# Kernel optimization log

Measured on AMD Instinct MI355X. Metric: run time of the kernel, lower is better.

The kernel has to match this reference:

```python
import jax, jax.numpy as jnp
import numpy as np

B, S, D, N = 8, 4096, 1024, 64
EPS = 1e-5


def setup_inputs() -> dict:
    key = jax.random.key(0)
    ks = jax.random.split(key, 6)
    sD = 1.0 / np.sqrt(D)
    sN = 1.0 / np.sqrt(N)
    return {
        "x": jax.random.normal(ks[0], (B, S, D), dtype=jnp.float32),
        "ln_w": jnp.ones((D,), jnp.float32),
        "ln_b": jnp.zeros((D,), jnp.float32),
        "Wi": jax.random.normal(ks[1], (N, D), jnp.float32) * sD,
        "bi": jnp.zeros((N,), jnp.float32),
        "Wf": jax.random.normal(ks[2], (N, D), jnp.float32) * sD,
        "bf": jnp.zeros((N,), jnp.float32),
        "Wz": jax.random.normal(ks[3], (N, D), jnp.float32) * sD,
        "bz": jnp.zeros((N,), jnp.float32),
        "Wo": jax.random.normal(ks[4], (N, D), jnp.float32) * sD,
        "bo": jnp.zeros((N,), jnp.float32),
        "Wp": jax.random.normal(ks[5], (D, N), jnp.float32) * sN,
        "bp": jnp.zeros((D,), jnp.float32),
    }


def reference(x, ln_w, ln_b, Wi, bi, Wf, bf, Wz, bz, Wo, bo, Wp, bp):
    # LayerNorm over last dim (eps matches torch default 1e-5)
    mu = jnp.mean(x, axis=-1, keepdims=True)
    var = jnp.mean(jnp.square(x - mu), axis=-1, keepdims=True)
    xn = (x - mu) * jax.lax.rsqrt(var + EPS) * ln_w + ln_b

    # Precompute all four projections as batched GEMMs: (B,S,N)
    log_i = jnp.clip(jnp.einsum('bsd,nd->bsn', xn, Wi) + bi, -20.0, 20.0)
    log_f = jnp.clip(jnp.einsum('bsd,nd->bsn', xn, Wf) + bf, -20.0, 20.0)
    z = jnp.tanh(jnp.einsum('bsd,nd->bsn', xn, Wz) + bz)
    o = jax.nn.sigmoid(jnp.einsum('bsd,nd->bsn', xn, Wo) + bo)

    # Stabilized exponential-gated recurrence via lax.scan over time
    def step(carry, inp):
        c, m = carry
        li, lf, zt, ot = inp
        m_new = jnp.maximum(m + lf, li)
        i_s = jnp.exp(li - m_new)
        f_s = jnp.exp(m + lf - m_new)
        c = f_s * c + i_s * zt
        h = ot * jnp.tanh(c)
        return (c, m_new), h

    c0 = jnp.zeros((x.shape[0], log_i.shape[-1]), x.dtype)
    m0 = jnp.zeros_like(c0)
    # time-major inputs: (S,B,N)
    tm = lambda a: jnp.swapaxes(a, 0, 1)
    _, h_seq = jax.lax.scan(step, (c0, m0), (tm(log_i), tm(log_f), tm(z), tm(o)))
    h_seq = jnp.swapaxes(h_seq, 0, 1)  # (B,S,N)

    return jnp.einsum('bsn,dn->bsd', h_seq, Wp) + bp
```

## Files before the change

### kernel.cpp

```cpp
#include <hip/hip_runtime.h>
#include <hip/hip_bf16.h>

#define BB 8
#define SS 4096
#define DD 1024
#define NN 64
#define ROWS (BB * SS)
#define GLD 256
#define NCHUNK 256
#define CLEN 16

typedef _Float16 f16;
using f16x8 = __attribute__((ext_vector_type(8))) _Float16;
using f32x4 = __attribute__((ext_vector_type(4))) float;

__global__ __launch_bounds__(256) void prep_all(const float* __restrict__ Wi, const float* __restrict__ bi,
                                                const float* __restrict__ Wf, const float* __restrict__ bfv,
                                                const float* __restrict__ Wz, const float* __restrict__ bz,
                                                const float* __restrict__ Wo, const float* __restrict__ bo,
                                                const float* __restrict__ Wp,
                                                const float* __restrict__ ln_w, const float* __restrict__ ln_b,
                                                f16* __restrict__ Wpk, f16* __restrict__ Wpf,
                                                float* __restrict__ ball, float* __restrict__ e_all) {
    if (blockIdx.x < 384) {
        int i = blockIdx.x * 256 + threadIdx.x;
        if (i < 32768) {
            int l = i & 63, cb = (i >> 6) & 15, s = i >> 10;
            int r = cb * 16 + (l & 15);
            int c = s * 32 + (l >> 4) * 8;
            int g = r >> 6, rem = r & 63;
            const float* W = (g == 0) ? Wi : (g == 1) ? Wf : (g == 2) ? Wz : Wo;
            const float* src = W + rem * 1024 + c;
            const float* lwp = ln_w + c;
            f16x8 v;
            #pragma unroll
            for (int e = 0; e < 8; ++e) v[e] = (f16)(src[e] * lwp[e]);
            *reinterpret_cast<f16x8*>(Wpk + (size_t)s * 8192 + cb * 512 + l * 8) = v;
        } else if (i < 32768 + 65536) {
            int j = i - 32768;
            Wpf[j] = (f16)Wp[j];
        }
    } else {
        int j = (blockIdx.x - 384) * 4 + (threadIdx.x >> 6);
        int lane = threadIdx.x & 63;
        int g = j >> 6, rem = j & 63;
        const float* W  = (g == 0) ? Wi : (g == 1) ? Wf : (g == 2) ? Wz : Wo;
        const float* bs = (g == 0) ? bi : (g == 1) ? bfv : (g == 2) ? bz : bo;
        const float* row = W + rem * 1024;
        float d = 0.0f, e = 0.0f;
        #pragma unroll
        for (int t = 0; t < 16; ++t) {
            int k = lane + 64 * t;
            float w = row[k];
            e += ln_w[k] * w;
            d += ln_b[k] * w;
        }
        #pragma unroll
        for (int off = 1; off < 64; off <<= 1) {
            e += __shfl_xor(e, off);
            d += __shfl_xor(d, off);
        }
        if (lane == 0) { ball[j] = bs[rem] + d; e_all[j] = e; }
    }
}

__global__ __launch_bounds__(512, 1) void gate_gemm(const float* __restrict__ x,
                                                    const f16* __restrict__ Wpk,
                                                    const float* __restrict__ ball,
                                                    const float* __restrict__ e_all,
                                                    float* __restrict__ gates,
                                                    float4* __restrict__ s4) {
    int bm = blockIdx.x * 128;
    int tid = threadIdx.x;
    int wid = tid >> 6, lane = tid & 63;
    int wm = wid >> 2, wn = wid & 3;
    int lrow = lane & 15, lkg = lane >> 4;
    int srow = tid >> 2, skg = tid & 3;

    __shared__ __align__(16) char ldsbuf[98304];
    __shared__ float2 stats_lds[128];

    const float4* xrow = reinterpret_cast<const float4*>(x + (size_t)(bm + srow) * DD) + skg * 4;
    float4 A0, A1, A2, A3, B0, B1, B2, B3;
    uint4 W0, W1, W2, W3;
    const uint4* wsrc = reinterpret_cast<const uint4*>(Wpk) + wid * 256 + lane;

    auto loadA = [&](int s) { const float4* p = xrow + s * 16; A0 = p[0]; A1 = p[1]; A2 = p[2]; A3 = p[3]; };
    auto loadB = [&](int s) { const float4* p = xrow + s * 16; B0 = p[0]; B1 = p[1]; B2 = p[2]; B3 = p[3]; };
    auto loadW = [&](int s) { const uint4* p = wsrc + (size_t)s * 2048; W0 = p[0]; W1 = p[64]; W2 = p[128]; W3 = p[192]; };
    auto writeW = [&](int buf) {
        uint4* d = reinterpret_cast<uint4*>(ldsbuf + buf * 32768 + wid * 4096) + lane;
        d[0] = W0; d[64] = W1; d[128] = W2; d[192] = W3;
    };

    float s1 = 0.0f, s2 = 0.0f;
    auto writeXv = [&](float4 v0, float4 v1, float4 v2, float4 v3, int buf) {
        float xv[16] = {v0.x, v0.y, v0.z, v0.w, v1.x, v1.y, v1.z, v1.w,
                        v2.x, v2.y, v2.z, v2.w, v3.x, v3.y, v3.z, v3.w};
        f16x8 p0, p1;
        #pragma unroll
        for (int e = 0; e < 8; ++e) {
            s1 += xv[e] + xv[8 + e];
            s2 += xv[e] * xv[e] + xv[8 + e] * xv[8 + e];
            p0[e] = (f16)xv[e];
            p1[e] = (f16)xv[8 + e];
        }
        char* base = ldsbuf + 65536 + buf * 16384 + srow * 128;
        int r7 = srow & 7;
        *reinterpret_cast<f16x8*>(base + 16 * ((2 * skg) ^ r7))     = p0;
        *reinterpret_cast<f16x8*>(base + 16 * ((2 * skg + 1) ^ r7)) = p1;
    };

    f32x4 acc[4][4] = {};
    auto compute = [&](int buf) {
        #pragma unroll
        for (int h = 0; h < 2; ++h) {
            f16x8 a[4];
            #pragma unroll
            for (int mf = 0; mf < 4; ++mf) {
                int row = wm * 64 + mf * 16 + lrow;
                a[mf] = *reinterpret_cast<const f16x8*>(
                    ldsbuf + 65536 + buf * 16384 + row * 128 + 16 * ((4 * h + lkg) ^ (row & 7)));
            }
            #pragma unroll
            for (int nf = 0; nf < 4; ++nf) {
                int cb = wn * 4 + nf;
                f16x8 w = *reinterpret_cast<const f16x8*>(
                    ldsbuf + buf * 32768 + h * 16384 + cb * 1024 + lane * 16);
                #pragma unroll
                for (int mf = 0; mf < 4; ++mf)
                    acc[mf][nf] = __builtin_amdgcn_mfma_f32_16x16x32_f16(a[mf], w, acc[mf][nf], 0, 0, 0);
            }
        }
    };
    auto stepSync = [&]() {
        asm volatile("s_waitcnt lgkmcnt(0)" ::: "memory");
        __builtin_amdgcn_s_barrier();
        __builtin_amdgcn_sched_barrier(0);
    };

    loadA(0); loadB(1); loadW(0);
    writeW(0);
    writeXv(A0, A1, A2, A3, 0);
    loadA(2); loadW(1);
    stepSync();

    for (int it = 0; it < 8; ++it) {
        int s = 2 * it;
        compute(0);
        writeW(1);
        writeXv(B0, B1, B2, B3, 1);
        if (s + 2 <= 15) loadW(s + 2);
        if (s + 3 <= 15) loadB(s + 3);
        stepSync();
        compute(1);
        if (s + 2 <= 15) {
            writeW(0);
            writeXv(A0, A1, A2, A3, 0);
        }
        if (s + 3 <= 15) loadW(s + 3);
        if (s + 4 <= 15) loadA(s + 4);
        stepSync();
    }

    s1 += __shfl_xor(s1, 1); s2 += __shfl_xor(s2, 1);
    s1 += __shfl_xor(s1, 2); s2 += __shfl_xor(s2, 2);
    if ((tid & 3) == 0) {
        float mu = s1 * (1.0f / DD);
        float var = s2 * (1.0f / DD) - mu * mu;
        float rsd = rsqrtf(var + 1e-5f);
        float2 st; st.x = mu * rsd; st.y = rsd;
        stats_lds[srow] = st;
    }
    __syncthreads();

    float* glds = reinterpret_cast<float*>(ldsbuf);
    int c0 = wn * 64;
    int rb = (lane >> 4) * 4;
    #pragma unroll
    for (int mf = 0; mf < 4; ++mf) {
        #pragma unroll
        for (int nf = 0; nf < 4; ++nf) {
            int col = c0 + nf * 16 + (lane & 15);
            float bc = ball[col];
            float ec = e_all[col];
            #pragma unroll
            for (int r = 0; r < 4; ++r) {
                int rl = wm * 64 + mf * 16 + rb + r;
                float2 st = stats_lds[rl];
                float v = acc[mf][nf][r] * st.y + bc - st.x * ec;
                float res;
                if (wn == 0 || wn == 1)      res = fminf(fmaxf(v, -20.0f), 20.0f);
                else if (wn == 2)            res = tanhf(v);
                else                         res = 1.0f / (1.0f + expf(-v));
                gates[(size_t)(bm + rl) * GLD + col] = res;
                if (wn < 3)
                    glds[rl * 192 + col] = res;
            }
        }
    }
    __syncthreads();

    int b = bm >> 12;
    int cb0 = (bm & 4095) >> 4;
    {
        int lr0 = wid * 16;
        float Lf = 0.0f, m = -1e30f, c = 0.0f;
        #pragma unroll
        for (int j = 0; j < 16; ++j) {
            const float* g = glds + (lr0 + j) * 192;
            float li = g[lane], lf = g[64 + lane], z = g[128 + lane];
            Lf += lf;
            float ma = m + lf;
            float mn = fmaxf(ma, li);
            c = __expf(ma - mn) * c + __expf(li - mn) * z;
            m = mn;
        }
        float4 v; v.x = Lf; v.y = m; v.z = c; v.w = 0.0f;
        s4[(size_t)(b * NCHUNK + cb0 + wid) * 64 + lane] = v;
    }
}

__global__ __launch_bounds__(64) void scan_b(const float4* __restrict__ s4,
                                             float2* __restrict__ c2) {
    int b = blockIdx.x;
    int n = threadIdx.x;
    size_t base = (size_t)b * NCHUNK * 64 + n;
    float c = 0.0f, m = 0.0f;
    float4 cur[16];
    #pragma unroll
    for (int d = 0; d < 16; ++d) cur[d] = s4[base + (size_t)d * 64];
    for (int kb = 0; kb < NCHUNK; kb += 16) {
        float4 nxt[16];
        if (kb + 16 < NCHUNK) {
            #pragma unroll
            for (int d = 0; d < 16; ++d) nxt[d] = s4[base + (size_t)(kb + 16 + d) * 64];
        }
        #pragma unroll
        for (int d = 0; d < 16; ++d) {
            float2 ci; ci.x = m; ci.y = c;
            c2[base + (size_t)(kb + d) * 64] = ci;
            float4 v = cur[d];
            float ma = m + v.x;
            float mo = fmaxf(ma, v.y);
            c = expf(ma - mo) * c + expf(v.y - mo) * v.z;
            m = mo;
        }
        #pragma unroll
        for (int d = 0; d < 16; ++d) cur[d] = nxt[d];
    }
}

__global__ __launch_bounds__(256) void out_fused(const float* __restrict__ gates,
                                                 const float2* __restrict__ c2,
                                                 const f16* __restrict__ Wpf,
                                                 const float* __restrict__ bp,
                                                 float* __restrict__ out) {
    int tid = threadIdx.x, wid = tid >> 6, lane = tid & 63;
    int r0 = blockIdx.x * 32;
    int b = r0 >> 12;
    int k0 = (r0 & 4095) >> 4;

    __shared__ __align__(16) f16 hlds[32 * 64];

    if (wid < 2) {
        int k = k0 + wid;
        float2 ci = c2[((size_t)b * NCHUNK + k) * 64 + lane];
        float m = ci.x, c = ci.y;
        const float* gp = gates + (size_t)(r0 + wid * 16) * GLD + lane;
        #pragma unroll
        for (int t = 0; t < 16; ++t) {
            float li = gp[0], lf = gp[64], z = gp[128], o = gp[192];
            gp += GLD;
            float ma = m + lf;
            float mn = fmaxf(ma, li);
            c = __expf(ma - mn) * c + __expf(li - mn) * z;
            m = mn;
            int row = wid * 16 + t;
            hlds[row * 64 + (((lane >> 3) ^ (row & 7)) << 3) + (lane & 7)] = (f16)(o * tanhf(c));
        }
    }
    __syncthreads();

    int c0 = wid * 256;
    int lrow = lane & 15, lkg = lane >> 4;
    f32x4 acc[2][16] = {};
    #pragma unroll
    for (int ks = 0; ks < 2; ++ks) {
        int kk = ks * 32;
        f16x8 a[2];
        #pragma unroll
        for (int mf = 0; mf < 2; ++mf) {
            int row = mf * 16 + lrow;
            int slot = (kk >> 3) + lkg;
            a[mf] = *reinterpret_cast<const f16x8*>(&hlds[row * 64 + ((slot ^ (row & 7)) << 3)]);
        }
        #pragma unroll
        for (int nf = 0; nf < 16; ++nf) {
            f16x8 bfr = *reinterpret_cast<const f16x8*>(Wpf + (size_t)(c0 + nf * 16 + lrow) * NN + kk + lkg * 8);
            #pragma unroll
            for (int mf = 0; mf < 2; ++mf)
                acc[mf][nf] = __builtin_amdgcn_mfma_f32_16x16x32_f16(a[mf], bfr, acc[mf][nf], 0, 0, 0);
        }
    }
    int rb = lkg * 4;
    #pragma unroll
    for (int nf = 0; nf < 16; ++nf) {
        int col = c0 + nf * 16 + lrow;
        float bias = bp[col];
        #pragma unroll
        for (int mf = 0; mf < 2; ++mf) {
            #pragma unroll
            for (int r = 0; r < 4; ++r) {
                int row = r0 + mf * 16 + rb + r;
                out[(size_t)row * DD + col] = acc[mf][nf][r] + bias;
            }
        }
    }
}

extern "C" void kernel_launch(void* const* d_in, const int* in_sizes, int n_in,
                              void* d_out, int out_size, void* d_ws, size_t ws_size,
                              hipStream_t stream) {
    const float* x    = (const float*)d_in[0];
    const float* ln_w = (const float*)d_in[1];
    const float* ln_b = (const float*)d_in[2];
    const float* Wi   = (const float*)d_in[3];
    const float* bi   = (const float*)d_in[4];
    const float* Wf   = (const float*)d_in[5];
    const float* bfv  = (const float*)d_in[6];
    const float* Wz   = (const float*)d_in[7];
    const float* bz   = (const float*)d_in[8];
    const float* Wo   = (const float*)d_in[9];
    const float* bo   = (const float*)d_in[10];
    const float* Wp   = (const float*)d_in[11];
    const float* bp   = (const float*)d_in[12];
    float* out = (float*)d_out;

    char* w = (char*)d_ws;
    float* gates = (float*)w;  w += (size_t)ROWS * GLD * 4;
    float4* s4   = (float4*)w; w += (size_t)BB * NCHUNK * 64 * 16;
    float2* c2   = (float2*)w; w += (size_t)BB * NCHUNK * 64 * 8;
    f16* Wpk     = (f16*)w;    w += 32 * 8192 * 2;
    f16* Wpf     = (f16*)w;    w += 1024 * 64 * 2;
    float* ball  = (float*)w;  w += 256 * 4;
    float* e_all = (float*)w;  w += 256 * 4;

    prep_all<<<448, 256, 0, stream>>>(Wi, bi, Wf, bfv, Wz, bz, Wo, bo, Wp,
                                      ln_w, ln_b, Wpk, Wpf, ball, e_all);
    gate_gemm<<<ROWS / 128, 512, 0, stream>>>(x, Wpk, ball, e_all, gates, s4);
    scan_b<<<BB, 64, 0, stream>>>(s4, c2);
    out_fused<<<ROWS / 32, 256, 0, stream>>>(gates, c2, Wpf, bp, out);
}
```

Measured before the change: 136.5 us.

## Split fused scan-and-output kernel into separate chunk-scan and output GEMM kernels

Replaces the fused out_fused kernel, where two of four waves ran the per-chunk recurrence into LDS before all waves did the output projection, with two kernels. scan_c runs the recurrence for each chunk and writes h to a new f16 workspace buffer. out_gemm then reads h from global memory and runs MFMA over half-width column tiles, launching twice as many blocks. This removes the idle waves during the serial scan phase and the LDS staging, at the cost of an extra kernel launch and a global round trip for h (about 4 MB).

```diff
diff --git a/kernel.cpp b/kernel.cpp
--- a/kernel.cpp
+++ b/kernel.cpp
@@ -251,62 +251,59 @@
     }
 }
 
-__global__ __launch_bounds__(256) void out_fused(const float* __restrict__ gates,
-                                                 const float2* __restrict__ c2,
-                                                 const f16* __restrict__ Wpf,
-                                                 const float* __restrict__ bp,
-                                                 float* __restrict__ out) {
+__global__ __launch_bounds__(256) void scan_c(const float* __restrict__ gates,
+                                              const float2* __restrict__ c2,
+                                              f16* __restrict__ h) {
+    int w = blockIdx.x * 4 + (threadIdx.x >> 6);
+    int lane = threadIdx.x & 63;
+    int b = w >> 8, k = w & (NCHUNK - 1);
+    int t0 = k * CLEN;
+    float2 ci = c2[(size_t)(b * NCHUNK + k) * 64 + lane];
+    float m = ci.x, c = ci.y;
+    const float* gp = gates + ((size_t)(b * SS + t0)) * GLD + lane;
+    f16* hp = h + ((size_t)(b * SS + t0)) * NN + lane;
+    for (int t = 0; t < CLEN; ++t) {
+        float li = gp[0], lf = gp[64], z = gp[128], o = gp[192];
+        gp += GLD;
+        float ma = m + lf;
+        float mn = fmaxf(ma, li);
+        c = expf(ma - mn) * c + expf(li - mn) * z;
+        m = mn;
+        *hp = (f16)(o * tanhf(c));
+        hp += NN;
+    }
+}
+
+__global__ __launch_bounds__(256) void out_gemm(const f16* __restrict__ h,
+                                                const f16* __restrict__ Wpf,
+                                                const float* __restrict__ bp,
+                                                float* __restrict__ out) {
     int tid = threadIdx.x, wid = tid >> 6, lane = tid & 63;
-    int r0 = blockIdx.x * 32;
-    int b = r0 >> 12;
-    int k0 = (r0 & 4095) >> 4;
-
-    __shared__ __align__(16) f16 hlds[32 * 64];
-
-    if (wid < 2) {
-        int k = k0 + wid;
-        float2 ci = c2[((size_t)b * NCHUNK + k) * 64 + lane];
-        float m = ci.x, c = ci.y;
-        const float* gp = gates + (size_t)(r0 + wid * 16) * GLD + lane;
-        #pragma unroll
-        for (int t = 0; t < 16; ++t) {
-            float li = gp[0], lf = gp[64], z = gp[128], o = gp[192];
-            gp += GLD;
-            float ma = m + lf;
-            float mn = fmaxf(ma, li);
-            c = __expf(ma - mn) * c + __expf(li - mn) * z;
-            m = mn;
-            int row = wid * 16 + t;
-            hlds[row * 64 + (((lane >> 3) ^ (row & 7)) << 3) + (lane & 7)] = (f16)(o * tanhf(c));
-        }
-    }
-    __syncthreads();
-
-    int c0 = wid * 256;
-    int lrow = lane & 15, lkg = lane >> 4;
-    f32x4 acc[2][16] = {};
+    int r0 = (blockIdx.x >> 1) * 32;
+    int c0 = (blockIdx.x & 1) * 512 + wid * 128;
+    int lrow = lane & 15, lk = (lane >> 4) * 8;
+
+    f32x4 acc[2][8] = {};
     #pragma unroll
     for (int ks = 0; ks < 2; ++ks) {
         int kk = ks * 32;
-        f16x8 a[2];
-        #pragma unroll
-        for (int mf = 0; mf < 2; ++mf) {
-            int row = mf * 16 + lrow;
-            int slot = (kk >> 3) + lkg;
-            a[mf] = *reinterpret_cast<const f16x8*>(&hlds[row * 64 + ((slot ^ (row & 7)) << 3)]);
-        }
-        #pragma unroll
-        for (int nf = 0; nf < 16; ++nf) {
-            f16x8 bfr = *reinterpret_cast<const f16x8*>(Wpf + (size_t)(c0 + nf * 16 + lrow) * NN + kk + lkg * 8);
-            #pragma unroll
-            for (int mf = 0; mf < 2; ++mf)
-                acc[mf][nf] = __builtin_amdgcn_mfma_f32_16x16x32_f16(a[mf], bfr, acc[mf][nf], 0, 0, 0);
-        }
-    }
-    int rb = lkg * 4;
+        f16x8 a[2], bfr[8];
+        #pragma unroll
+        for (int mf = 0; mf < 2; ++mf)
+            a[mf] = *reinterpret_cast<const f16x8*>(h + (size_t)(r0 + mf * 16 + lrow) * NN + kk + lk);
+        #pragma unroll
+        for (int nf = 0; nf < 8; ++nf)
+            bfr[nf] = *reinterpret_cast<const f16x8*>(Wpf + (size_t)(c0 + nf * 16 + lrow) * NN + kk + lk);
+        #pragma unroll
+        for (int mf = 0; mf < 2; ++mf)
+            #pragma unroll
+            for (int nf = 0; nf < 8; ++nf)
+                acc[mf][nf] = __builtin_amdgcn_mfma_f32_16x16x32_f16(a[mf], bfr[nf], acc[mf][nf], 0, 0, 0);
+    }
+    int rb = (lane >> 4) * 4;
     #pragma unroll
-    for (int nf = 0; nf < 16; ++nf) {
-        int col = c0 + nf * 16 + lrow;
+    for (int nf = 0; nf < 8; ++nf) {
+        int col = c0 + nf * 16 + (lane & 15);
         float bias = bp[col];
         #pragma unroll
         for (int mf = 0; mf < 2; ++mf) {
@@ -341,6 +338,7 @@
     float* gates = (float*)w;  w += (size_t)ROWS * GLD * 4;
     float4* s4   = (float4*)w; w += (size_t)BB * NCHUNK * 64 * 16;
     float2* c2   = (float2*)w; w += (size_t)BB * NCHUNK * 64 * 8;
+    f16* h       = (f16*)w;    w += (size_t)ROWS * NN * 2;
     f16* Wpk     = (f16*)w;    w += 32 * 8192 * 2;
     f16* Wpf     = (f16*)w;    w += 1024 * 64 * 2;
     float* ball  = (float*)w;  w += 256 * 4;
@@ -350,5 +348,6 @@
                                       ln_w, ln_b, Wpk, Wpf, ball, e_all);
     gate_gemm<<<ROWS / 128, 512, 0, stream>>>(x, Wpk, ball, e_all, gates, s4);
     scan_b<<<BB, 64, 0, stream>>>(s4, c2);
-    out_fused<<<ROWS / 32, 256, 0, stream>>>(gates, c2, Wpf, bp, out);
-}
+    scan_c<<<(BB * NCHUNK) / 4, 256, 0, stream>>>(gates, c2, h);
+    out_gemm<<<(ROWS / 32) * 2, 256, 0, stream>>>(h, Wpf, bp, out);
+}
```

Measured after the change: 139.7 us. +2.3%, slower.
